# Performance work log

Measured on AMD Instinct MI355X. Metric: run time of the kernel, lower is better.

The kernel has to match this reference:

```python
import jax, jax.numpy as jnp
import numpy as np

N = 100000          # number of nodes (queries == sources here)
DEG = 32            # uniform neighbor count
E = N * DEG         # total edges
C_IN = 8
HID = 32
C_OUT = 32


def setup_inputs() -> dict:
    key = jax.random.key(0)
    k1, k2, k3, k4, k5 = jax.random.split(key, 5)
    in_features = jax.random.normal(k1, (N, C_IN), dtype=jnp.float32)
    in_weights = jax.random.uniform(k2, (N,), dtype=jnp.float32)
    # MLP: Linear(2*C_IN -> HID), GELU, Linear(HID -> C_OUT)
    W1 = jax.random.normal(k3, (2 * C_IN, HID), dtype=jnp.float32) / np.sqrt(2 * C_IN)
    b1 = jnp.zeros((HID,), dtype=jnp.float32)
    W2 = jax.random.normal(k4, (HID, C_OUT), dtype=jnp.float32) / np.sqrt(HID)
    b2 = jnp.zeros((C_OUT,), dtype=jnp.float32)
    neighbor_index = jax.random.randint(k5, (E,), 0, N, dtype=jnp.int64)
    row_splits = (jnp.arange(N + 1, dtype=jnp.int64) * DEG)  # uniform CSR splits
    return {"in_features": in_features, "in_weights": in_weights,
            "W1": W1, "b1": b1, "W2": W2, "b2": b2,
            "neighbor_index": neighbor_index, "row_splits": row_splits}


def reference(in_features, in_weights, W1, b1, W2, b2, neighbor_index, row_splits):
    num_edges = neighbor_index.shape[0]
    num_out = row_splits.shape[0] - 1  # M output nodes
    # segment id of each edge (== repeat_interleave of node ids by row counts)
    seg = jnp.searchsorted(row_splits, jnp.arange(num_edges), side="right") - 1
    gathered = in_features[neighbor_index]          # [E, C_in] neighbor gather
    self_feats = in_features[seg]                   # [E, C_in] repeated self features
    agg = jnp.concatenate([gathered, self_feats], axis=1)  # [E, 2*C_in]
    h = jax.nn.gelu(agg @ W1 + b1)                  # [E, HID]
    h = h @ W2 + b2                                 # [E, C_out]
    h = in_weights[neighbor_index][:, None] * h     # quadrature weighting
    sums = jax.ops.segment_sum(h, seg, num_segments=num_out)  # segment_csr sum
    counts = (row_splits[1:] - row_splits[:-1]).astype(h.dtype)
    out = sums / jnp.maximum(counts, 1)[:, None]    # reduce='mean'
    return out
```

## Files before the change

kernel.cpp:

```cpp
#include <hip/hip_runtime.h>

#define DEG 32
#define HID 32
#define CIN 8

typedef float v2f __attribute__((ext_vector_type(2)));
typedef short bf16x8 __attribute__((ext_vector_type(8)));
typedef float f32x16 __attribute__((ext_vector_type(16)));

#define GELU_A ((float)(2.0 * 1.4426950408889634 * 0.7978845608028654))
#define GELU_B ((float)(2.0 * 1.4426950408889634 * 0.7978845608028654 * 0.044715))

__device__ __forceinline__ unsigned f2bf(float f) {
    unsigned b = __float_as_uint(f);
    return (b + 0x7fffu + ((b >> 16) & 1u)) >> 16;
}
__device__ __forceinline__ unsigned pack2(float lo, float hi) {
    return f2bf(lo) | (f2bf(hi) << 16);
}

__global__ __launch_bounds__(256) void precompute_xw(
    const float* __restrict__ x, const float* __restrict__ W1,
    const float* __restrict__ W2, unsigned* __restrict__ x16,
    unsigned* __restrict__ w1f, unsigned* __restrict__ w2f, int N) {
    int tid = blockIdx.x * 256 + threadIdx.x;
    if (blockIdx.x == 0) {
        int t = threadIdx.x;
        if (t < 64) {
            int kb = (t >> 5) * 8, col = t & 31;
            uint4 o;
            o.x = pack2(W1[(kb + 0) * HID + col], W1[(kb + 1) * HID + col]);
            o.y = pack2(W1[(kb + 2) * HID + col], W1[(kb + 3) * HID + col]);
            o.z = pack2(W1[(kb + 4) * HID + col], W1[(kb + 5) * HID + col]);
            o.w = pack2(W1[(kb + 6) * HID + col], W1[(kb + 7) * HID + col]);
            *(uint4*)(w1f + t * 4) = o;
        } else if (t < 192) {
            int u = t - 64;
            int f = u >> 6, l = u & 63;
            int kb = f * 16 + ((l >> 5) * 8), col = l & 31;
            uint4 o;
            o.x = pack2(W2[(kb + 0) * HID + col], W2[(kb + 1) * HID + col]);
            o.y = pack2(W2[(kb + 2) * HID + col], W2[(kb + 3) * HID + col]);
            o.z = pack2(W2[(kb + 4) * HID + col], W2[(kb + 5) * HID + col]);
            o.w = pack2(W2[(kb + 6) * HID + col], W2[(kb + 7) * HID + col]);
            *(uint4*)(w2f + (f * 64 + l) * 4) = o;
        }
    }
    if (tid < N) {
        const float4* xp = (const float4*)(x + (size_t)tid * CIN);
        float4 a = xp[0], b = xp[1];
        uint4 o;
        o.x = pack2(a.x, a.y);  o.y = pack2(a.z, a.w);
        o.z = pack2(b.x, b.y);  o.w = pack2(b.z, b.w);
        *(uint4*)(x16 + (size_t)tid * 4) = o;
    }
}

__device__ __forceinline__ float gelu_reduce(const f32x16& acc, const float* swp,
                                             float b1v) {
    float4 wq0 = *(const float4*)(swp);
    float4 wq1 = *(const float4*)(swp + 8);
    float4 wq2 = *(const float4*)(swp + 16);
    float4 wq3 = *(const float4*)(swp + 24);
    float wqa[16] = {wq0.x, wq0.y, wq0.z, wq0.w,  wq1.x, wq1.y, wq1.z, wq1.w,
                     wq2.x, wq2.y, wq2.z, wq2.w,  wq3.x, wq3.y, wq3.z, wq3.w};
    v2f gacc = {0.f, 0.f};
#pragma unroll
    for (int i = 0; i < 16; i += 2) {
        v2f tt = {acc[i] + b1v, acc[i + 1] + b1v};
        v2f x2 = tt * tt;
        v2f zz = tt * (x2 * (-GELU_B) + (-GELU_A));
        v2f ee;
        ee.x = __builtin_amdgcn_exp2f(zz.x);  ee.y = __builtin_amdgcn_exp2f(zz.y);
        v2f dd = ee + 1.0f;
        v2f rr;
        rr.x = __builtin_amdgcn_rcpf(dd.x);   rr.y = __builtin_amdgcn_rcpf(dd.y);
        v2f wp = {wqa[i], wqa[i + 1]};
        gacc += wp * (tt * rr);
    }
    float g = gacc.x + gacc.y;
    g += __shfl_xor(g, 32);
    return g;
}

__global__ __launch_bounds__(256, 5) void git_fused(
    const unsigned* __restrict__ x16, const unsigned* __restrict__ w1f,
    const unsigned* __restrict__ w2f, const float* __restrict__ wgt,
    const float* __restrict__ b1, const float* __restrict__ b2,
    const int* __restrict__ nbr, float* __restrict__ out, int N) {
    __shared__ float          sw[8 * DEG];
    __shared__ unsigned short sg[32 * 40];
    __shared__ float          sws[32];

    int t = threadIdx.x;
    int wv = t >> 6;
    int l  = t & 63;
    int l5 = l & 31;
    int hi = l >> 5;
    int nb = blockIdx.x * 8 + wv * 2;

    int jn[2]; float w[2]; int ncl[2];
#pragma unroll
    for (int r = 0; r < 2; ++r) {
        int n = nb + r; ncl[r] = n < N ? n : (N - 1);
        jn[r] = nbr[ncl[r] * DEG + l5];
        w[r]  = wgt[jn[r]];
    }
    if (hi == 0) {
#pragma unroll
        for (int r = 0; r < 2; ++r) sw[(wv * 2 + r) * DEG + l5] = w[r];
    }

    float ws[2];
#pragma unroll
    for (int r = 0; r < 2; ++r) {
        float s = w[r];
        s += __shfl_xor(s, 1);  s += __shfl_xor(s, 2);
        s += __shfl_xor(s, 4);  s += __shfl_xor(s, 8);
        s += __shfl_xor(s, 16);
        ws[r] = s;
    }

    bf16x8 af0 = *((const bf16x8*)x16 + (hi ? ncl[0] : jn[0]));
    bf16x8 af1 = *((const bf16x8*)x16 + (hi ? ncl[1] : jn[1]));
    bf16x8 bf  = *((const bf16x8*)w1f + l);
    float myb1 = b1[l5];

    f32x16 z0 = {}, z1 = {};
    f32x16 a0 = __builtin_amdgcn_mfma_f32_32x32x16_bf16(af0, bf, z0, 0, 0, 0);
    f32x16 a1 = __builtin_amdgcn_mfma_f32_32x32x16_bf16(af1, bf, z1, 0, 0, 0);

    const float* swb = &sw[wv * 2 * DEG + hi * 4];
    float g0 = gelu_reduce(a0, swb, myb1);
    float g1 = gelu_reduce(a1, swb + DEG, myb1);

    if (hi == 0) {
        sg[(wv * 2 + 0) * 40 + l5] = (unsigned short)f2bf(g0);
        sg[(wv * 2 + 1) * 40 + l5] = (unsigned short)f2bf(g1);
        if (l5 == 0) { sws[wv * 2] = ws[0]; sws[wv * 2 + 1] = ws[1]; }
    }

    __syncthreads();

    if (wv != 0) return;

    const char* sgb = (const char*)sg;
    bf16x8 ea1 = *(const bf16x8*)(sgb + l5 * 80 + hi * 16);
    bf16x8 ea2 = *(const bf16x8*)(sgb + l5 * 80 + 32 + hi * 16);
    bf16x8 eb1 = *((const bf16x8*)w2f + l);
    bf16x8 eb2 = *((const bf16x8*)w2f + 64 + l);

    f32x16 zz = {};
    f32x16 acc = __builtin_amdgcn_mfma_f32_32x32x16_bf16(ea1, eb1, zz, 0, 0, 0);
    acc = __builtin_amdgcn_mfma_f32_32x32x16_bf16(ea2, eb2, acc, 0, 0, 0);

    float myb2 = b2[l5];
    float4 wsq = *(const float4*)(sws + hi * 4);
    float wsa[4] = {wsq.x, wsq.y, wsq.z, wsq.w};

#pragma unroll
    for (int i = 0; i < 4; ++i) {
        int r = i + 4 * hi;
        int node = blockIdx.x * 8 + r;
        if (node < N)
            out[(size_t)node * HID + l5] = fmaf(wsa[i], myb2, acc[i]) * (1.0f / DEG);
    }
}

__global__ __launch_bounds__(256) void fused_fallback(
    const float* __restrict__ x, const float* __restrict__ wgt,
    const float* __restrict__ W1, const float* __restrict__ b1,
    const float* __restrict__ W2, const float* __restrict__ b2,
    const int* __restrict__ nbr, float* __restrict__ out, int N) {
    __shared__ float sW2[HID * HID];
    __shared__ float sb2[HID];
    __shared__ int2  sp[8 * DEG];
    int t = threadIdx.x;
#pragma unroll
    for (int i = 0; i < 4; ++i) sW2[t + i * 256] = W2[t + i * 256];
    if (t < HID) sb2[t] = b2[t];
    int slot = t >> 5, hid = t & 31;
    int node = blockIdx.x * 8 + slot;
    bool valid = node < N;
    int nc = valid ? node : (N - 1);
    int   j_own = nbr[nc * DEG + hid];
    float w_own = wgt[j_own];
    sp[slot * DEG + hid] = make_int2(j_own * (CIN * 4), __float_as_int(w_own));
    const float4* xip = (const float4*)(x + (size_t)nc * CIN);
    float4 xa = xip[0], xb = xip[1];
    float w1t[8];
#pragma unroll
    for (int k = 0; k < 8; ++k) w1t[k] = W1[k * HID + hid];
    float vb = b1[hid];
    vb = fmaf(xa.x, W1[ 8 * HID + hid], vb);
    vb = fmaf(xa.y, W1[ 9 * HID + hid], vb);
    vb = fmaf(xa.z, W1[10 * HID + hid], vb);
    vb = fmaf(xa.w, W1[11 * HID + hid], vb);
    vb = fmaf(xb.x, W1[12 * HID + hid], vb);
    vb = fmaf(xb.y, W1[13 * HID + hid], vb);
    vb = fmaf(xb.z, W1[14 * HID + hid], vb);
    vb = fmaf(xb.w, W1[15 * HID + hid], vb);
    float ws = w_own;
    ws += __shfl_xor(ws, 1);  ws += __shfl_xor(ws, 2);
    ws += __shfl_xor(ws, 4);  ws += __shfl_xor(ws, 8);
    ws += __shfl_xor(ws, 16);
    __syncthreads();
    const char* xbytes = (const char*)x;
    const int2* myp = &sp[slot * DEG];
    float g = 0.f;
#pragma unroll 8
    for (int e = 0; e < DEG; ++e) {
        int2  p  = myp[e];
        float wjv = __int_as_float(p.y);
        const float4* xjp = (const float4*)(xbytes + (unsigned)p.x);
        float4 a = xjp[0], b = xjp[1];
        float tin = vb;
        tin = fmaf(a.x, w1t[0], tin); tin = fmaf(a.y, w1t[1], tin);
        tin = fmaf(a.z, w1t[2], tin); tin = fmaf(a.w, w1t[3], tin);
        tin = fmaf(b.x, w1t[4], tin); tin = fmaf(b.y, w1t[5], tin);
        tin = fmaf(b.z, w1t[6], tin); tin = fmaf(b.w, w1t[7], tin);
        float x2 = tin * tin;
        float z  = tin * fmaf(GELU_B, x2, GELU_A);
        float e2 = __builtin_amdgcn_exp2f(z);
        float r  = __builtin_amdgcn_rcpf(1.0f + e2);
        g = fmaf(wjv, fmaf(-tin, r, tin), g);
    }
    float acc = 0.f;
#pragma unroll
    for (int h = 0; h < HID; ++h) {
        float gh = __shfl(g, h, 32);
        acc = fmaf(gh, sW2[h * HID + hid], acc);
    }
    if (valid) out[(size_t)node * HID + hid] = fmaf(ws, sb2[hid], acc) * (1.0f / DEG);
}

extern "C" void kernel_launch(void* const* d_in, const int* in_sizes, int n_in,
                              void* d_out, int out_size, void* d_ws, size_t ws_size,
                              hipStream_t stream) {
    const float* x   = (const float*)d_in[0];
    const float* wq  = (const float*)d_in[1];
    const float* W1  = (const float*)d_in[2];
    const float* b1  = (const float*)d_in[3];
    const float* W2  = (const float*)d_in[4];
    const float* b2  = (const float*)d_in[5];
    const int*   nbr = (const int*)d_in[6];
    float* out = (float*)d_out;

    int N = in_sizes[1];

    size_t off_x16 = 0;
    size_t off_w1  = (off_x16 + (size_t)N * 16 + 255) & ~(size_t)255;
    size_t off_w2  = off_w1 + 1024;
    size_t need    = off_w2 + 2048;

    if (ws_size >= need) {
        unsigned* x16 = (unsigned*)((char*)d_ws + off_x16);
        unsigned* w1f = (unsigned*)((char*)d_ws + off_w1);
        unsigned* w2f = (unsigned*)((char*)d_ws + off_w2);

        int blocks_pre = (N + 255) / 256;
        precompute_xw<<<blocks_pre, 256, 0, stream>>>(x, W1, W2, x16, w1f, w2f, N);

        int blocks_main = (N + 7) / 8;
        git_fused<<<blocks_main, 256, 0, stream>>>(x16, w1f, w2f, wq, b1, b2,
                                                   nbr, out, N);
    } else {
        int blocks = (N + 7) / 8;
        fused_fallback<<<blocks, 256, 0, stream>>>(x, wq, W1, b1, W2, b2, nbr, out, N);
    }
}
```

Before: 114.3 us.

## Make second MLP layer per-wave to drop block barrier

Each wave now computes the second-layer MFMA for its own two nodes from wave-local shared memory, instead of one wave doing all eight nodes after a __syncthreads. This removes the block-wide barrier and the idle waves that returned early. It also raises the occupancy hint from 5 to 6 blocks per CU. The cost is that every wave issues two extra MFMAs that use only 2 of 32 rows, plus W2 fragment loads. Reading shared memory written by other lanes of the same wave with no explicit wave barrier leans on lockstep execution.

```diff
diff --git a/kernel.cpp b/kernel.cpp
--- a/kernel.cpp
+++ b/kernel.cpp
@@ -83,14 +83,13 @@
     return g;
 }
 
-__global__ __launch_bounds__(256, 5) void git_fused(
+__global__ __launch_bounds__(256, 6) void git_fused2(
     const unsigned* __restrict__ x16, const unsigned* __restrict__ w1f,
     const unsigned* __restrict__ w2f, const float* __restrict__ wgt,
     const float* __restrict__ b1, const float* __restrict__ b2,
     const int* __restrict__ nbr, float* __restrict__ out, int N) {
-    __shared__ float          sw[8 * DEG];
-    __shared__ unsigned short sg[32 * 40];
-    __shared__ float          sws[32];
+    __shared__ float          sw[4][2 * DEG];
+    __shared__ unsigned short sg[4][2 * 32];
 
     int t = threadIdx.x;
     int wv = t >> 6;
@@ -108,62 +107,57 @@
     }
     if (hi == 0) {
 #pragma unroll
-        for (int r = 0; r < 2; ++r) sw[(wv * 2 + r) * DEG + l5] = w[r];
-    }
-
-    float ws[2];
-#pragma unroll
-    for (int r = 0; r < 2; ++r) {
-        float s = w[r];
+        for (int r = 0; r < 2; ++r) sw[wv][r * DEG + l5] = w[r];
+    }
+
+    float ws0, ws1;
+    {
+        float s = w[0];
         s += __shfl_xor(s, 1);  s += __shfl_xor(s, 2);
         s += __shfl_xor(s, 4);  s += __shfl_xor(s, 8);
         s += __shfl_xor(s, 16);
-        ws[r] = s;
+        ws0 = s;
+        s = w[1];
+        s += __shfl_xor(s, 1);  s += __shfl_xor(s, 2);
+        s += __shfl_xor(s, 4);  s += __shfl_xor(s, 8);
+        s += __shfl_xor(s, 16);
+        ws1 = s;
     }
 
     bf16x8 af0 = *((const bf16x8*)x16 + (hi ? ncl[0] : jn[0]));
     bf16x8 af1 = *((const bf16x8*)x16 + (hi ? ncl[1] : jn[1]));
     bf16x8 bf  = *((const bf16x8*)w1f + l);
+    bf16x8 eb1 = *((const bf16x8*)w2f + l);
+    bf16x8 eb2 = *((const bf16x8*)w2f + 64 + l);
     float myb1 = b1[l5];
+    float myb2 = b2[l5];
 
     f32x16 z0 = {}, z1 = {};
     f32x16 a0 = __builtin_amdgcn_mfma_f32_32x32x16_bf16(af0, bf, z0, 0, 0, 0);
     f32x16 a1 = __builtin_amdgcn_mfma_f32_32x32x16_bf16(af1, bf, z1, 0, 0, 0);
 
-    const float* swb = &sw[wv * 2 * DEG + hi * 4];
+    const float* swb = &sw[wv][hi * 4];
     float g0 = gelu_reduce(a0, swb, myb1);
     float g1 = gelu_reduce(a1, swb + DEG, myb1);
 
     if (hi == 0) {
-        sg[(wv * 2 + 0) * 40 + l5] = (unsigned short)f2bf(g0);
-        sg[(wv * 2 + 1) * 40 + l5] = (unsigned short)f2bf(g1);
-        if (l5 == 0) { sws[wv * 2] = ws[0]; sws[wv * 2 + 1] = ws[1]; }
-    }
-
-    __syncthreads();
-
-    if (wv != 0) return;
-
-    const char* sgb = (const char*)sg;
-    bf16x8 ea1 = *(const bf16x8*)(sgb + l5 * 80 + hi * 16);
-    bf16x8 ea2 = *(const bf16x8*)(sgb + l5 * 80 + 32 + hi * 16);
-    bf16x8 eb1 = *((const bf16x8*)w2f + l);
-    bf16x8 eb2 = *((const bf16x8*)w2f + 64 + l);
+        sg[wv][l5]      = (unsigned short)f2bf(g0);
+        sg[wv][32 + l5] = (unsigned short)f2bf(g1);
+    }
+    int arow = l5 < 2 ? l5 : 1;
+    const unsigned short* sgw = &sg[wv][0];
+    bf16x8 ea1 = *(const bf16x8*)(sgw + arow * 32 + hi * 8);
+    bf16x8 ea2 = *(const bf16x8*)(sgw + arow * 32 + 16 + hi * 8);
 
     f32x16 zz = {};
     f32x16 acc = __builtin_amdgcn_mfma_f32_32x32x16_bf16(ea1, eb1, zz, 0, 0, 0);
     acc = __builtin_amdgcn_mfma_f32_32x32x16_bf16(ea2, eb2, acc, 0, 0, 0);
 
-    float myb2 = b2[l5];
-    float4 wsq = *(const float4*)(sws + hi * 4);
-    float wsa[4] = {wsq.x, wsq.y, wsq.z, wsq.w};
-
-#pragma unroll
-    for (int i = 0; i < 4; ++i) {
-        int r = i + 4 * hi;
-        int node = blockIdx.x * 8 + r;
-        if (node < N)
-            out[(size_t)node * HID + l5] = fmaf(wsa[i], myb2, acc[i]) * (1.0f / DEG);
+    if (hi == 0) {
+        if (nb < N)
+            out[(size_t)nb * HID + l5]       = fmaf(ws0, myb2, acc[0]) * (1.0f / DEG);
+        if (nb + 1 < N)
+            out[(size_t)(nb + 1) * HID + l5] = fmaf(ws1, myb2, acc[1]) * (1.0f / DEG);
     }
 }
 
@@ -262,8 +256,8 @@
         precompute_xw<<<blocks_pre, 256, 0, stream>>>(x, W1, W2, x16, w1f, w2f, N);
 
         int blocks_main = (N + 7) / 8;
-        git_fused<<<blocks_main, 256, 0, stream>>>(x16, w1f, w2f, wq, b1, b2,
-                                                   nbr, out, N);
+        git_fused2<<<blocks_main, 256, 0, stream>>>(x16, w1f, w2f, wq, b1, b2,
+                                                    nbr, out, N);
     } else {
         int blocks = (N + 7) / 8;
         fused_fallback<<<blocks, 256, 0, stream>>>(x, wq, W1, b1, W2, b2, nbr, out, N);
```

After: 114.7 us. Within noise of the previous version (+0.4%).
